# Kernel optimization log

Measured on AMD Instinct MI355X. Metric: run time of the kernel, lower is better.

The kernel has to match this reference:

```python
import jax, jax.numpy as jnp
import numpy as np

N = 100000
E = 1600000
GENE = 512
HID = 128
NCLS = 10
EPS = 1e-5  # BatchNorm1d default eps


def setup_inputs() -> dict:
    key = jax.random.key(0)
    ks = jax.random.split(key, 16)
    def lin(k, fan_in, fan_out):
        return (jax.random.normal(k, (fan_in, fan_out), jnp.float32) / np.sqrt(fan_in)).astype(jnp.float32)
    dims = [(GENE, HID), (HID, 2 * HID), (2 * HID, HID), (HID, HID // 2)]
    inp = {}
    inp["x"] = jax.random.normal(ks[0], (N, GENE), jnp.float32)
    inp["edge_index"] = jax.random.randint(ks[1], (2, E), 0, N)
    for i, (di, do) in enumerate(dims, start=1):
        inp[f"W{i}"] = lin(ks[1 + i], di, do)
        inp[f"b{i}"] = jnp.zeros((do,), jnp.float32)
        inp[f"g{i}"] = jnp.ones((do,), jnp.float32)     # BN gamma
        inp[f"beta{i}"] = jnp.zeros((do,), jnp.float32)  # BN beta
    inp["Wc"] = lin(ks[10], HID // 2, NCLS)
    inp["bc"] = jnp.zeros((NCLS,), jnp.float32)
    return inp


def gcn_conv(h_in, W, b, src, dst, deg_inv_sqrt):
    # PyG GCNConv: transform, then symmetric-normalized aggregation with self-loops
    h = h_in @ W                                   # [N, out]
    norm = (deg_inv_sqrt[src] * deg_inv_sqrt[dst])[:, None]  # [E, 1]
    agg = jnp.zeros_like(h).at[dst].add(h[src] * norm)       # scatter-add over edges
    agg = agg + h * (deg_inv_sqrt ** 2)[:, None]   # self-loop contribution (norm = 1/deg)
    return agg + b


def relu_bn(h, g, beta):
    # forward applies BatchNorm1d(F.relu(h)) in training mode (batch stats, biased var)
    h = jax.nn.relu(h)
    mu = h.mean(axis=0)
    var = h.var(axis=0)
    return (h - mu) * jax.lax.rsqrt(var + EPS) * g + beta


def reference(x, edge_index, W1, b1, g1, beta1, W2, b2, g2, beta2,
              W3, b3, g3, beta3, W4, b4, g4, beta4, Wc, bc):
    src, dst = edge_index[0], edge_index[1]
    # degree after adding self-loops (edge weight 1)
    deg = jnp.zeros((x.shape[0],), x.dtype).at[dst].add(1.0) + 1.0
    dis = jax.lax.rsqrt(deg)
    h = relu_bn(gcn_conv(x, W1, b1, src, dst, dis), g1, beta1)
    h = relu_bn(gcn_conv(h, W2, b2, src, dst, dis), g2, beta2)
    h = relu_bn(gcn_conv(h, W3, b3, src, dst, dis), g3, beta3)
    h = relu_bn(gcn_conv(h, W4, b4, src, dst, dis), g4, beta4)
    return h @ Wc + bc
```

## Files before the change

### kernel.cpp

```cpp
#include <hip/hip_runtime.h>
#include <hip/hip_bf16.h>

#define EPS_BN 1e-5f

using frag8 = __attribute__((ext_vector_type(8))) short;
using f32x4 = __attribute__((ext_vector_type(4))) float;

typedef const __attribute__((address_space(1))) void* gas_ptr;
typedef __attribute__((address_space(3))) void* las_ptr;

__device__ __forceinline__ void async_ld16(const void* g, void* l) {
  __builtin_amdgcn_global_load_lds((gas_ptr)g, (las_ptr)l, 16, 0, 0);
}

__device__ __forceinline__ float bfu2f(unsigned short u) {
  union { unsigned int i; float f; } c;
  c.i = (unsigned int)u << 16;
  return c.f;
}


__global__ void wtrans1_kernel(const float* __restrict__ W1, __hip_bfloat16* __restrict__ T) {
  int i = blockIdx.x * blockDim.x + threadIdx.x;
  if (i < 512 * 128) {
    int k = i / 128, f = i % 128;
    T[f * 512 + k] = __float2bfloat16(W1[i]);
  }
}

__global__ void scan1_kernel(const int* __restrict__ cnt, int* __restrict__ out,
                             int* __restrict__ bsum, float* __restrict__ dis, int n) {
  __shared__ int sdata[1024];
  int tid = threadIdx.x;
  int i = blockIdx.x * 1024 + tid;
  int v = (i < n) ? cnt[i] : 0;
  if (i < n) dis[i] = rsqrtf((float)v + 1.0f);
  sdata[tid] = v;
  __syncthreads();
  for (int off = 1; off < 1024; off <<= 1) {
    int t = (tid >= off) ? sdata[tid - off] : 0;
    __syncthreads();
    sdata[tid] += t;
    __syncthreads();
  }
  if (i < n) out[i] = sdata[tid] - v;
  if (tid == 1023) bsum[blockIdx.x] = sdata[1023];
}

__global__ void scan2_kernel(int* __restrict__ bsum, int nb) {
  __shared__ int sdata[1024];
  int tid = threadIdx.x;
  int v = (tid < nb) ? bsum[tid] : 0;
  sdata[tid] = v;
  __syncthreads();
  for (int off = 1; off < 1024; off <<= 1) {
    int t = (tid >= off) ? sdata[tid - off] : 0;
    __syncthreads();
    sdata[tid] += t;
    __syncthreads();
  }
  if (tid < nb) bsum[tid] = sdata[tid] - v;
}

__global__ void scan3_kernel(int* __restrict__ out, const int* __restrict__ bsum,
                             int n, int E) {
  int i = blockIdx.x * 1024 + threadIdx.x;
  if (i < n) out[i] += bsum[blockIdx.x];
  if (i == 0) out[n] = E;
}

template <int TN, int ASTAGE, int OMODE>
__device__ __forceinline__ void gemm_body(
    const void* __restrict__ Ap, const __hip_bfloat16* __restrict__ Bt,
    __hip_bfloat16* __restrict__ C, const float* __restrict__ bias,
    const float* __restrict__ rowscale,
    const float* __restrict__ statsIn, const float* __restrict__ g,
    const float* __restrict__ beta, float* __restrict__ statsOut, float invN,
    int Nr, int K, int F, int bx, int by) {
  constexpr int WM = (TN == 128) ? 64 : 32;
  constexpr int MI = WM / 16;
  __shared__ __align__(16) __hip_bfloat16 As[128 * 32];
  __shared__ __align__(16) __hip_bfloat16 Bs[TN * 32];
  __shared__ float sacc[128], sqc[128];
  __shared__ float ssc[256], ssb[256];
  int tid = (int)threadIdx.x;
  int wid = tid >> 6, lane = tid & 63;
  int rowBase = bx * 128;
  int colBase = by * TN;
  int wr, wc;
  if (TN == 128) { wr = (wid >> 1) * 64; wc = (wid & 1) * 64; }
  else           { wr = wid * 32;        wc = 0; }

  f32x4 zero = {0.f, 0.f, 0.f, 0.f};
  f32x4 acc[MI][4];
#pragma unroll
  for (int i = 0; i < MI; ++i)
#pragma unroll
    for (int j = 0; j < 4; ++j) acc[i][j] = zero;

  int lm = lane & 15;
  int k8 = (lane >> 4) * 8;

  if constexpr (OMODE == 3) {
    if (tid < 128) { sacc[tid] = 0.f; sqc[tid] = 0.f; }
  }
  if constexpr (ASTAGE == 2) {
    for (int k = tid; k < K; k += 256) {
      float mean = statsIn[k] * invN;
      float var = statsIn[256 + k] * invN - mean * mean;
      float sc = g[k] * rsqrtf(var + EPS_BN);
      ssc[k] = sc;
      ssb[k] = beta[k] - mean * sc;
    }
    __syncthreads();
  }

  for (int k0 = 0; k0 < K; k0 += 32) {
    if constexpr (ASTAGE == 0) {
#pragma unroll
      for (int p = 0; p < 2; ++p) {
        int sidx = p * 256 + tid;
        int row = sidx >> 2;
        int kq = (sidx & 3) * 8;
        int gr = rowBase + row;
        if (gr >= Nr) gr = Nr - 1;
        async_ld16((const __hip_bfloat16*)Ap + (size_t)gr * K + k0 + kq,
                   (char*)As + (p * 256 + wid * 64) * 16);
      }
    } else {
#pragma unroll
      for (int p = 0; p < 2; ++p) {
        int sidx = p * 256 + tid;
        int row = sidx >> 2;
        int kq = (sidx & 3) * 8;
        int gr = rowBase + row;
        if (gr >= Nr) gr = Nr - 1;
        union { frag8 f; __hip_bfloat16 h[8]; } pk;
        if constexpr (ASTAGE == 1) {
          const float* s = (const float*)Ap + (size_t)gr * K + k0 + kq;
          float4 a = *(const float4*)s;
          float4 b2 = *(const float4*)(s + 4);
          pk.h[0] = __float2bfloat16(a.x);  pk.h[1] = __float2bfloat16(a.y);
          pk.h[2] = __float2bfloat16(a.z);  pk.h[3] = __float2bfloat16(a.w);
          pk.h[4] = __float2bfloat16(b2.x); pk.h[5] = __float2bfloat16(b2.y);
          pk.h[6] = __float2bfloat16(b2.z); pk.h[7] = __float2bfloat16(b2.w);
        } else {
          const unsigned short* s = (const unsigned short*)Ap + (size_t)gr * K + k0 + kq;
          ushort4 a = *(const ushort4*)s;
          ushort4 b2 = *(const ushort4*)(s + 4);
          int kk = k0 + kq;
          pk.h[0] = __float2bfloat16(bfu2f(a.x)  * ssc[kk + 0] + ssb[kk + 0]);
          pk.h[1] = __float2bfloat16(bfu2f(a.y)  * ssc[kk + 1] + ssb[kk + 1]);
          pk.h[2] = __float2bfloat16(bfu2f(a.z)  * ssc[kk + 2] + ssb[kk + 2]);
          pk.h[3] = __float2bfloat16(bfu2f(a.w)  * ssc[kk + 3] + ssb[kk + 3]);
          pk.h[4] = __float2bfloat16(bfu2f(b2.x) * ssc[kk + 4] + ssb[kk + 4]);
          pk.h[5] = __float2bfloat16(bfu2f(b2.y) * ssc[kk + 5] + ssb[kk + 5]);
          pk.h[6] = __float2bfloat16(bfu2f(b2.z) * ssc[kk + 6] + ssb[kk + 6]);
          pk.h[7] = __float2bfloat16(bfu2f(b2.w) * ssc[kk + 7] + ssb[kk + 7]);
        }
        *(frag8*)&As[row * 32 + kq] = pk.f;
      }
    }
    constexpr int BPASS = TN / 64;
#pragma unroll
    for (int p = 0; p < BPASS; ++p) {
      int sidx = p * 256 + tid;
      int col = sidx >> 2;
      int kq = (sidx & 3) * 8;
      async_ld16(Bt + (size_t)(colBase + col) * K + k0 + kq,
                 (char*)Bs + (p * 256 + wid * 64) * 16);
    }
    __syncthreads();

    frag8 af[MI], bf[4];
#pragma unroll
    for (int i = 0; i < MI; ++i)
      af[i] = *(const frag8*)&As[(wr + i * 16 + lm) * 32 + k8];
#pragma unroll
    for (int j = 0; j < 4; ++j)
      bf[j] = *(const frag8*)&Bs[(wc + j * 16 + lm) * 32 + k8];
#pragma unroll
    for (int i = 0; i < MI; ++i)
#pragma unroll
      for (int j = 0; j < 4; ++j)
        acc[i][j] = __builtin_amdgcn_mfma_f32_16x16x32_bf16(af[i], bf[j], acc[i][j], 0, 0, 0);
    __syncthreads();
  }

  int rquad = (lane >> 4) * 4;
  float s[4] = {0.f, 0.f, 0.f, 0.f}, q[4] = {0.f, 0.f, 0.f, 0.f};
#pragma unroll
  for (int i = 0; i < MI; ++i) {
    int rb = rowBase + wr + i * 16 + rquad;
#pragma unroll
    for (int r = 0; r < 4; ++r) {
      int row = rb + r;
      if (row < Nr) {
        if constexpr (OMODE == 0) {
#pragma unroll
          for (int j = 0; j < 4; ++j) {
            int col = colBase + wc + j * 16 + lm;
            C[(size_t)row * F + col] = __float2bfloat16(acc[i][j][r]);
          }
        } else if constexpr (OMODE == 1) {
          float rs = rowscale[row];
#pragma unroll
          for (int j = 0; j < 4; ++j) {
            int col = colBase + wc + j * 16 + lm;
            C[(size_t)row * F + col] = __float2bfloat16(acc[i][j][r] * rs);
          }
        } else {
#pragma unroll
          for (int j = 0; j < 4; ++j) {
            int col = colBase + wc + j * 16 + lm;
            float v = acc[i][j][r] + bias[col];
            float rl = fmaxf(v, 0.f);
            C[(size_t)row * F + col] = __float2bfloat16(rl);
            s[j] += rl;
            q[j] += rl * rl;
          }
        }
      }
    }
  }

  if constexpr (OMODE == 3) {
#pragma unroll
    for (int j = 0; j < 4; ++j) {
      s[j] += __shfl_xor(s[j], 16, 64); s[j] += __shfl_xor(s[j], 32, 64);
      q[j] += __shfl_xor(q[j], 16, 64); q[j] += __shfl_xor(q[j], 32, 64);
    }
    if (lane < 16) {
#pragma unroll
      for (int j = 0; j < 4; ++j) {
        atomicAdd(&sacc[wc + j * 16 + lane], s[j]);
        atomicAdd(&sqc[wc + j * 16 + lane], q[j]);
      }
    }
    __syncthreads();
    if (tid < 128) {
      atomicAdd(&statsOut[colBase + tid], sacc[tid]);
      atomicAdd(&statsOut[256 + colBase + tid], sqc[tid]);
    }
  }
}

__global__ __launch_bounds__(256) void fat1_kernel(
    const float* __restrict__ x, const __hip_bfloat16* __restrict__ Wt0,
    __hip_bfloat16* __restrict__ T1, int Nn, int G1,
    const int* __restrict__ e_dst, int* __restrict__ cnt, int* __restrict__ rank,
    int E, int CB,
    const float* __restrict__ W2, const float* __restrict__ W3, const float* __restrict__ W4,
    __hip_bfloat16* __restrict__ Tw2, __hip_bfloat16* __restrict__ Tw3,
    __hip_bfloat16* __restrict__ Tw4) {
  int b = (int)blockIdx.x;
  if (b < G1) {
    gemm_body<128, 1, 0>(x, Wt0, T1, nullptr, nullptr, nullptr, nullptr, nullptr,
                         nullptr, 0.f, Nn, 512, 128, b, 0);
  } else if (b < G1 + CB) {
    int e = (b - G1) * 256 + (int)threadIdx.x;
    if (e < E) rank[e] = atomicAdd(&cnt[e_dst[e]], 1);
  } else {
    int i = (b - G1 - CB) * 256 + (int)threadIdx.x;
    const float* W; __hip_bfloat16* T; int K, F, base;
    if (i < 32768)       { W = W2; T = Tw2; K = 128; F = 256; base = 0; }
    else if (i < 65536)  { W = W3; T = Tw3; K = 256; F = 128; base = 32768; }
    else if (i < 73728)  { W = W4; T = Tw4; K = 128; F = 64;  base = 65536; }
    else return;
    int j = i - base;
    int k = j / F, f = j % F;
    T[f * K + k] = __float2bfloat16(W[j]);
  }
}

template <int TN, int ASTAGE, int OMODE>
__global__ __launch_bounds__(256) void mfma_gemm_kernel(
    const void* __restrict__ A, const __hip_bfloat16* __restrict__ Bt,
    __hip_bfloat16* __restrict__ C, const float* __restrict__ bias,
    const float* __restrict__ rowscale, const float* __restrict__ statsIn,
    const float* __restrict__ g, const float* __restrict__ beta,
    float* __restrict__ statsOut, float invN, int Nr, int K, int F) {
  gemm_body<TN, ASTAGE, OMODE>(A, Bt, C, bias, rowscale, statsIn, g, beta, statsOut,
                               invN, Nr, K, F, (int)blockIdx.x, (int)blockIdx.y);
}

__global__ __launch_bounds__(256) void fat2_kernel(
    const int* __restrict__ src, const int* __restrict__ dst,
    const int* __restrict__ rowstart, const int* __restrict__ rank,
    int* __restrict__ csr_src, int E) {
  int e = (int)blockIdx.x * 256 + (int)threadIdx.x;
  if (e < E) csr_src[rowstart[dst[e]] + rank[e]] = src[e];
}

template <int VEC, int AMODE>
__global__ __launch_bounds__(256) void agg_kernel(
    const __hip_bfloat16* __restrict__ Ts, const int* __restrict__ rowstart,
    const int* __restrict__ csr_src, const float* __restrict__ dis,
    const float* __restrict__ bias, void* __restrict__ H,
    float* __restrict__ stats, const float* __restrict__ statsIn,
    const float* __restrict__ g, const float* __restrict__ beta,
    float* __restrict__ sd, float invN, int Nn, int F) {
  __shared__ float lsum[512], lqs[512];
  __shared__ float ssc[128], ssb[128];
  int tid = (int)threadIdx.x;
  int wid4 = tid >> 6;
  int lane = tid & 63;
  int off = lane * VEC;
  const unsigned short* Tu = (const unsigned short*)Ts;

  if constexpr (AMODE == 2) {
    if (tid < F) {
      float mean = statsIn[tid] * invN;
      float var = statsIn[256 + tid] * invN - mean * mean;
      float sc = g[tid] * rsqrtf(var + EPS_BN);
      ssc[tid] = sc;
      ssb[tid] = beta[tid] - mean * sc;
    }
    __syncthreads();
  }

  float bj[VEC];
  float s[VEC], q[VEC];
#pragma unroll
  for (int j = 0; j < VEC; ++j) {
    bj[j] = (AMODE == 1 || AMODE == 3 || AMODE == 4) ? bias[off + j] : 0.f;
    s[j] = 0.f; q[j] = 0.f;
  }

  for (int d = blockIdx.x * 4 + wid4; d < Nn; d += gridDim.x * 4) {
    float dd = dis[d];
    float acc[VEC];
    {
      unsigned short r[VEC];
      if constexpr (VEC == 2) *(ushort2*)r = *(const ushort2*)&Tu[(size_t)d * F + off];
      else                    r[0] = Tu[(size_t)d * F + off];
#pragma unroll
      for (int j = 0; j < VEC; ++j) {
        if constexpr (AMODE == 1) acc[j] = bfu2f(r[j]) * dd;
        else                      acc[j] = bfu2f(r[j]);
      }
    }
    float sdacc = dd;

    int e0 = rowstart[d], e1 = rowstart[d + 1];
    for (int e = e0; e < e1; e += 16) {
      int idx[16];
      bool val[16];
#pragma unroll
      for (int p = 0; p < 16; ++p) {
        int ee = e + p;
        val[p] = ee < e1;
        idx[p] = csr_src[val[p] ? ee : e1 - 1];
      }
      unsigned short r[16][VEC];
      float dv[16];
#pragma unroll
      for (int p = 0; p < 16; ++p) {
        if constexpr (VEC == 2) *(ushort2*)r[p] = *(const ushort2*)&Tu[(size_t)idx[p] * F + off];
        else                    r[p][0] = Tu[(size_t)idx[p] * F + off];
        if constexpr (AMODE == 1) dv[p] = dis[idx[p]];
      }
#pragma unroll
      for (int p = 0; p < 16; ++p) {
        if constexpr (AMODE == 1) {
#pragma unroll
          for (int j = 0; j < VEC; ++j) acc[j] += val[p] ? bfu2f(r[p][j]) * dv[p] : 0.f;
          sdacc += val[p] ? dv[p] : 0.f;
        } else {
#pragma unroll
          for (int j = 0; j < VEC; ++j) acc[j] += val[p] ? bfu2f(r[p][j]) : 0.f;
        }
      }
    }

    if constexpr (AMODE == 2) {
      float sdv = sd[d];
      union { ushort2 u; __hip_bfloat16 h[2]; } pk;
      pk.h[0] = __float2bfloat16(dd * (ssc[off + 0] * acc[0] + ssb[off + 0] * sdv));
      pk.h[1] = __float2bfloat16(dd * (ssc[off + 1] * acc[1] + ssb[off + 1] * sdv));
      *(ushort2*)&((__hip_bfloat16*)H)[(size_t)d * F + off] = pk.u;
    } else {
      float rl[VEC];
#pragma unroll
      for (int j = 0; j < VEC; ++j) {
        float v = acc[j] * dd + bj[j];
        rl[j] = fmaxf(v, 0.f);
        s[j] += rl[j];
        q[j] += rl[j] * rl[j];
      }
      if constexpr (AMODE == 1) {
        union { ushort2 u; __hip_bfloat16 h[2]; } pk;
        pk.h[0] = __float2bfloat16(rl[0] * dd);
        pk.h[1] = __float2bfloat16(rl[1] * dd);
        *(ushort2*)&((__hip_bfloat16*)H)[(size_t)d * F + off] = pk.u;
        if (lane == 0) sd[d] = sdacc;
      } else if constexpr (AMODE == 3) {
        union { ushort2 u; __hip_bfloat16 h[2]; } pk;
        pk.h[0] = __float2bfloat16(rl[0]);
        pk.h[1] = __float2bfloat16(rl[1]);
        *(ushort2*)&((__hip_bfloat16*)H)[(size_t)d * F + off] = pk.u;
      } else {
        ((float*)H)[(size_t)d * F + off] = rl[0];
      }
    }
  }

  if constexpr (AMODE != 2) {
#pragma unroll
    for (int j = 0; j < VEC; ++j) {
      lsum[(lane * VEC + j) * 4 + wid4] = s[j];
      lqs[(lane * VEC + j) * 4 + wid4] = q[j];
    }
    __syncthreads();
    int nc = 64 * VEC;
    for (int c = tid; c < nc; c += 256) {
      float a = lsum[c * 4 + 0] + lsum[c * 4 + 1] + lsum[c * 4 + 2] + lsum[c * 4 + 3];
      float b = lqs[c * 4 + 0] + lqs[c * 4 + 1] + lqs[c * 4 + 2] + lqs[c * 4 + 3];
      atomicAdd(&stats[c], a);
      atomicAdd(&stats[256 + c], b);
    }
  }
}

__global__ __launch_bounds__(256) void bnapply_cls_kernel(
    const float* __restrict__ R4, const float* __restrict__ stats,
    const float* __restrict__ g, const float* __restrict__ beta,
    const float* __restrict__ Wc, const float* __restrict__ bc,
    float* __restrict__ out, int Nn, float invN) {
  __shared__ float ssc[64], ssb[64];
  int tid = (int)threadIdx.x;
  if (tid < 64) {
    float mean = stats[tid] * invN;
    float var = stats[256 + tid] * invN - mean * mean;
    float sc = g[tid] * rsqrtf(var + EPS_BN);
    ssc[tid] = sc;
    ssb[tid] = beta[tid] - mean * sc;
  }
  __syncthreads();
  int gt = blockIdx.x * blockDim.x + tid;
  int wid = gt >> 6;
  int lane = tid & 63;
  if (wid >= Nn) return;
  float v = R4[(size_t)wid * 64 + lane];
  float h = v * ssc[lane] + ssb[lane];
#pragma unroll
  for (int c = 0; c < 10; ++c) {
    float p = h * Wc[lane * 10 + c];
#pragma unroll
    for (int off = 32; off > 0; off >>= 1) p += __shfl_down(p, off, 64);
    if (lane == 0) out[(size_t)wid * 10 + c] = p + bc[c];
  }
}


extern "C" void kernel_launch(void* const* d_in, const int* in_sizes, int n_in,
                              void* d_out, int out_size, void* d_ws, size_t ws_size,
                              hipStream_t stream) {
  (void)n_in; (void)out_size; (void)ws_size;
  const float* x    = (const float*)d_in[0];
  const int*   edge = (const int*)d_in[1];
  const int E  = in_sizes[1] / 2;
  const int Nn = in_sizes[0] / 512;
  const int* e_src = edge;
  const int* e_dst = edge + E;

  const float* W[4]  = {(const float*)d_in[2],  (const float*)d_in[6],
                        (const float*)d_in[10], (const float*)d_in[14]};
  const float* bv[4] = {(const float*)d_in[3],  (const float*)d_in[7],
                        (const float*)d_in[11], (const float*)d_in[15]};
  const float* gv[4] = {(const float*)d_in[4],  (const float*)d_in[8],
                        (const float*)d_in[12], (const float*)d_in[16]};
  const float* bt[4] = {(const float*)d_in[5],  (const float*)d_in[9],
                        (const float*)d_in[13], (const float*)d_in[17]};
  const float* Wc = (const float*)d_in[18];
  const float* bc = (const float*)d_in[19];
  float* out = (float*)d_out;

  const float invN = 1.0f / (float)Nn;

  char* p = (char*)d_ws;
  auto alloc = [&](size_t bytes) -> void* {
    void* r = (void*)p;
    p += (bytes + 255) & ~(size_t)255;
    return r;
  };
  int*   cnt      = (int*)alloc((size_t)Nn * 4);
  float* stats    = (float*)alloc(2048 * 4);
  size_t zeroBytes = (size_t)(((size_t)Nn * 4 + 255) & ~(size_t)255) + 2048 * 4;
  int*   rowstart = (int*)alloc((size_t)(Nn + 1) * 4);
  int*   bsum     = (int*)alloc(1024 * 4);
  float* dis      = (float*)alloc((size_t)Nn * 4);
  float* sd       = (float*)alloc((size_t)Nn * 4);
  int*   rank     = (int*)alloc((size_t)E * 4);
  int*   csr_src  = (int*)alloc((size_t)E * 4);
  __hip_bfloat16* Wt0 = (__hip_bfloat16*)alloc(512 * 128 * 2);
  __hip_bfloat16* Wt1 = (__hip_bfloat16*)alloc(128 * 256 * 2);
  __hip_bfloat16* Wt2 = (__hip_bfloat16*)alloc(256 * 128 * 2);
  __hip_bfloat16* Wt3 = (__hip_bfloat16*)alloc(128 * 64 * 2);
  __hip_bfloat16* Ts1 = (__hip_bfloat16*)alloc((size_t)Nn * 128 * 2);
  __hip_bfloat16* R1  = (__hip_bfloat16*)alloc((size_t)Nn * 128 * 2);
  __hip_bfloat16* Tb2 = (__hip_bfloat16*)alloc((size_t)Nn * 128 * 2);
  __hip_bfloat16* R2  = (__hip_bfloat16*)alloc((size_t)Nn * 256 * 2);
  __hip_bfloat16* Ts3 = (__hip_bfloat16*)alloc((size_t)Nn * 128 * 2);
  __hip_bfloat16* R3  = (__hip_bfloat16*)alloc((size_t)Nn * 128 * 2);
  __hip_bfloat16* Ts4 = (__hip_bfloat16*)alloc((size_t)Nn * 64 * 2);
  float*          R4  = (float*)alloc((size_t)Nn * 64 * 4);

  hipMemsetAsync(cnt, 0, zeroBytes, stream);

  wtrans1_kernel<<<(512 * 128 + 255) / 256, 256, 0, stream>>>(W[0], Wt0);

  const int gx = (Nn + 127) / 128;
  const int CB = (E + 255) / 256;
  const int WB = (73728 + 255) / 256;
  fat1_kernel<<<gx + CB + WB, 256, 0, stream>>>(
      x, Wt0, Ts1, Nn, gx, e_dst, cnt, rank, E, CB,
      W[1], W[2], W[3], Wt1, Wt2, Wt3);

  int nb = (Nn + 1023) / 1024;
  scan1_kernel<<<nb, 1024, 0, stream>>>(cnt, rowstart, bsum, dis, Nn);
  scan2_kernel<<<1, 1024, 0, stream>>>(bsum, nb);
  scan3_kernel<<<nb, 1024, 0, stream>>>(rowstart, bsum, Nn, E);

  fat2_kernel<<<CB, 256, 0, stream>>>(e_src, e_dst, rowstart, rank, csr_src, E);

  const int AGG_BLOCKS = 2048;

  agg_kernel<2, 1><<<AGG_BLOCKS, 256, 0, stream>>>(
      Ts1, rowstart, csr_src, dis, bv[0], R1, stats, nullptr, nullptr, nullptr,
      sd, invN, Nn, 128);
  agg_kernel<2, 2><<<AGG_BLOCKS, 256, 0, stream>>>(
      R1, rowstart, csr_src, dis, nullptr, Tb2, nullptr, stats, gv[0], bt[0],
      sd, invN, Nn, 128);
  {
    dim3 g(gx, 2);
    mfma_gemm_kernel<128, 0, 3><<<g, 256, 0, stream>>>(
        Tb2, Wt1, R2, bv[1], nullptr, nullptr, nullptr, nullptr, stats + 512, invN,
        Nn, 128, 256);
  }
  {
    dim3 g(gx, 1);
    mfma_gemm_kernel<128, 2, 1><<<g, 256, 0, stream>>>(
        R2, Wt2, Ts3, nullptr, dis, stats + 512, gv[1], bt[1], nullptr, invN,
        Nn, 256, 128);
  }
  agg_kernel<2, 3><<<AGG_BLOCKS, 256, 0, stream>>>(
      Ts3, rowstart, csr_src, dis, bv[2], R3, stats + 1024, nullptr, nullptr, nullptr,
      nullptr, invN, Nn, 128);
  {
    dim3 g(gx, 1);
    mfma_gemm_kernel<64, 2, 1><<<g, 256, 0, stream>>>(
        R3, Wt3, Ts4, nullptr, dis, stats + 1024, gv[2], bt[2], nullptr, invN,
        Nn, 128, 64);
  }
  agg_kernel<1, 4><<<AGG_BLOCKS, 256, 0, stream>>>(
      Ts4, rowstart, csr_src, dis, bv[3], R4, stats + 1536, nullptr, nullptr, nullptr,
      nullptr, invN, Nn, 64);
  int clsBlocks = (Nn * 64 + 255) / 256;
  bnapply_cls_kernel<<<clsBlocks, 256, 0, stream>>>(R4, stats + 1536, gv[3], bt[3],
                                                    Wc, bc, out, Nn, invN);
}
```

Measured before the change: 940.0 us.

## Double-buffer GEMM shared-memory tiles to overlap next-tile loads with MFMA

Converts the GEMM K-loop into a two-stage software pipeline. As and Bs are now double-buffered, and the loads for tile t+1 are issued before the MFMAs on tile t. Register-staged A tiles (fp32 convert, BN affine) are converted and stored after the compute. The loop drops from two barriers per iteration to one and hoists the address computation out of the loop. In exchange it doubles shared-memory use and adds prefetch registers, which may lower occupancy.

```diff
diff --git a/kernel.cpp b/kernel.cpp
--- a/kernel.cpp
+++ b/kernel.cpp
@@ -79,8 +79,9 @@
     int Nr, int K, int F, int bx, int by) {
   constexpr int WM = (TN == 128) ? 64 : 32;
   constexpr int MI = WM / 16;
-  __shared__ __align__(16) __hip_bfloat16 As[128 * 32];
-  __shared__ __align__(16) __hip_bfloat16 Bs[TN * 32];
+  constexpr int BPASS = TN / 64;
+  __shared__ __align__(16) __hip_bfloat16 As[2][128 * 32];
+  __shared__ __align__(16) __hip_bfloat16 Bs[2][TN * 32];
   __shared__ float sacc[128], sqc[128];
   __shared__ float ssc[256], ssb[256];
   int tid = (int)threadIdx.x;
@@ -101,6 +102,26 @@
   int lm = lane & 15;
   int k8 = (lane >> 4) * 8;
 
+  int arow[2], alrow[2], akq[2], adst[2];
+#pragma unroll
+  for (int p = 0; p < 2; ++p) {
+    int sidx = p * 256 + tid;
+    alrow[p] = sidx >> 2;
+    akq[p] = (sidx & 3) * 8;
+    int gr = rowBase + alrow[p];
+    if (gr >= Nr) gr = Nr - 1;
+    arow[p] = gr;
+    adst[p] = (p * 256 + wid * 64) * 16;
+  }
+  int bcol[BPASS], bkq[BPASS], bdst[BPASS];
+#pragma unroll
+  for (int p = 0; p < BPASS; ++p) {
+    int sidx = p * 256 + tid;
+    bcol[p] = colBase + (sidx >> 2);
+    bkq[p] = (sidx & 3) * 8;
+    bdst[p] = (p * 256 + wid * 64) * 16;
+  }
+
   if constexpr (OMODE == 3) {
     if (tid < 128) { sacc[tid] = 0.f; sqc[tid] = 0.f; }
   }
@@ -115,76 +136,109 @@
     __syncthreads();
   }
 
-  for (int k0 = 0; k0 < K; k0 += 32) {
-    if constexpr (ASTAGE == 0) {
-#pragma unroll
-      for (int p = 0; p < 2; ++p) {
-        int sidx = p * 256 + tid;
-        int row = sidx >> 2;
-        int kq = (sidx & 3) * 8;
-        int gr = rowBase + row;
-        if (gr >= Nr) gr = Nr - 1;
-        async_ld16((const __hip_bfloat16*)Ap + (size_t)gr * K + k0 + kq,
-                   (char*)As + (p * 256 + wid * 64) * 16);
-      }
-    } else {
-#pragma unroll
-      for (int p = 0; p < 2; ++p) {
-        int sidx = p * 256 + tid;
-        int row = sidx >> 2;
-        int kq = (sidx & 3) * 8;
-        int gr = rowBase + row;
-        if (gr >= Nr) gr = Nr - 1;
-        union { frag8 f; __hip_bfloat16 h[8]; } pk;
-        if constexpr (ASTAGE == 1) {
-          const float* s = (const float*)Ap + (size_t)gr * K + k0 + kq;
-          float4 a = *(const float4*)s;
-          float4 b2 = *(const float4*)(s + 4);
-          pk.h[0] = __float2bfloat16(a.x);  pk.h[1] = __float2bfloat16(a.y);
-          pk.h[2] = __float2bfloat16(a.z);  pk.h[3] = __float2bfloat16(a.w);
-          pk.h[4] = __float2bfloat16(b2.x); pk.h[5] = __float2bfloat16(b2.y);
-          pk.h[6] = __float2bfloat16(b2.z); pk.h[7] = __float2bfloat16(b2.w);
-        } else {
-          const unsigned short* s = (const unsigned short*)Ap + (size_t)gr * K + k0 + kq;
-          ushort4 a = *(const ushort4*)s;
-          ushort4 b2 = *(const ushort4*)(s + 4);
-          int kk = k0 + kq;
-          pk.h[0] = __float2bfloat16(bfu2f(a.x)  * ssc[kk + 0] + ssb[kk + 0]);
-          pk.h[1] = __float2bfloat16(bfu2f(a.y)  * ssc[kk + 1] + ssb[kk + 1]);
-          pk.h[2] = __float2bfloat16(bfu2f(a.z)  * ssc[kk + 2] + ssb[kk + 2]);
-          pk.h[3] = __float2bfloat16(bfu2f(a.w)  * ssc[kk + 3] + ssb[kk + 3]);
-          pk.h[4] = __float2bfloat16(bfu2f(b2.x) * ssc[kk + 4] + ssb[kk + 4]);
-          pk.h[5] = __float2bfloat16(bfu2f(b2.y) * ssc[kk + 5] + ssb[kk + 5]);
-          pk.h[6] = __float2bfloat16(bfu2f(b2.z) * ssc[kk + 6] + ssb[kk + 6]);
-          pk.h[7] = __float2bfloat16(bfu2f(b2.w) * ssc[kk + 7] + ssb[kk + 7]);
+  auto cvt_store_f32 = [&](int p, int buf, float4 a, float4 b2) {
+    union { frag8 f; __hip_bfloat16 h[8]; } pk;
+    pk.h[0] = __float2bfloat16(a.x);  pk.h[1] = __float2bfloat16(a.y);
+    pk.h[2] = __float2bfloat16(a.z);  pk.h[3] = __float2bfloat16(a.w);
+    pk.h[4] = __float2bfloat16(b2.x); pk.h[5] = __float2bfloat16(b2.y);
+    pk.h[6] = __float2bfloat16(b2.z); pk.h[7] = __float2bfloat16(b2.w);
+    *(frag8*)&As[buf][alrow[p] * 32 + akq[p]] = pk.f;
+  };
+  auto cvt_store_bn = [&](int p, int buf, int kk, ushort4 a, ushort4 b2) {
+    union { frag8 f; __hip_bfloat16 h[8]; } pk;
+    pk.h[0] = __float2bfloat16(bfu2f(a.x)  * ssc[kk + 0] + ssb[kk + 0]);
+    pk.h[1] = __float2bfloat16(bfu2f(a.y)  * ssc[kk + 1] + ssb[kk + 1]);
+    pk.h[2] = __float2bfloat16(bfu2f(a.z)  * ssc[kk + 2] + ssb[kk + 2]);
+    pk.h[3] = __float2bfloat16(bfu2f(a.w)  * ssc[kk + 3] + ssb[kk + 3]);
+    pk.h[4] = __float2bfloat16(bfu2f(b2.x) * ssc[kk + 4] + ssb[kk + 4]);
+    pk.h[5] = __float2bfloat16(bfu2f(b2.y) * ssc[kk + 5] + ssb[kk + 5]);
+    pk.h[6] = __float2bfloat16(bfu2f(b2.z) * ssc[kk + 6] + ssb[kk + 6]);
+    pk.h[7] = __float2bfloat16(bfu2f(b2.w) * ssc[kk + 7] + ssb[kk + 7]);
+    *(frag8*)&As[buf][alrow[p] * 32 + akq[p]] = pk.f;
+  };
+
+  if constexpr (ASTAGE == 0) {
+#pragma unroll
+    for (int p = 0; p < 2; ++p)
+      async_ld16((const __hip_bfloat16*)Ap + (size_t)arow[p] * K + akq[p],
+                 (char*)As[0] + adst[p]);
+  } else if constexpr (ASTAGE == 1) {
+#pragma unroll
+    for (int p = 0; p < 2; ++p) {
+      const float* s = (const float*)Ap + (size_t)arow[p] * K + akq[p];
+      cvt_store_f32(p, 0, *(const float4*)s, *(const float4*)(s + 4));
+    }
+  } else {
+#pragma unroll
+    for (int p = 0; p < 2; ++p) {
+      const unsigned short* s = (const unsigned short*)Ap + (size_t)arow[p] * K + akq[p];
+      cvt_store_bn(p, 0, akq[p], *(const ushort4*)s, *(const ushort4*)(s + 4));
+    }
+  }
+#pragma unroll
+  for (int p = 0; p < BPASS; ++p)
+    async_ld16(Bt + (size_t)bcol[p] * K + bkq[p], (char*)Bs[0] + bdst[p]);
+  __syncthreads();
+
+  int nt = K >> 5;
+  int cur = 0;
+  for (int t = 0; t < nt; ++t) {
+    int k0n = (t + 1) << 5;
+    bool hasNext = (t + 1) < nt;
+    float4 pf0[2], pf1[2];
+    ushort4 pu0[2], pu1[2];
+
+    if (hasNext) {
+      if constexpr (ASTAGE == 0) {
+#pragma unroll
+        for (int p = 0; p < 2; ++p)
+          async_ld16((const __hip_bfloat16*)Ap + (size_t)arow[p] * K + k0n + akq[p],
+                     (char*)As[cur ^ 1] + adst[p]);
+      } else if constexpr (ASTAGE == 1) {
+#pragma unroll
+        for (int p = 0; p < 2; ++p) {
+          const float* s = (const float*)Ap + (size_t)arow[p] * K + k0n + akq[p];
+          pf0[p] = *(const float4*)s;
+          pf1[p] = *(const float4*)(s + 4);
         }
-        *(frag8*)&As[row * 32 + kq] = pk.f;
-      }
-    }
-    constexpr int BPASS = TN / 64;
-#pragma unroll
-    for (int p = 0; p < BPASS; ++p) {
-      int sidx = p * 256 + tid;
-      int col = sidx >> 2;
-      int kq = (sidx & 3) * 8;
-      async_ld16(Bt + (size_t)(colBase + col) * K + k0 + kq,
-                 (char*)Bs + (p * 256 + wid * 64) * 16);
-    }
-    __syncthreads();
-
-    frag8 af[MI], bf[4];
+      } else {
+#pragma unroll
+        for (int p = 0; p < 2; ++p) {
+          const unsigned short* s =
+              (const unsigned short*)Ap + (size_t)arow[p] * K + k0n + akq[p];
+          pu0[p] = *(const ushort4*)s;
+          pu1[p] = *(const ushort4*)(s + 4);
+        }
+      }
+#pragma unroll
+      for (int p = 0; p < BPASS; ++p)
+        async_ld16(Bt + (size_t)bcol[p] * K + k0n + bkq[p], (char*)Bs[cur ^ 1] + bdst[p]);
+    }
+
+    frag8 af[MI], bfr[4];
 #pragma unroll
     for (int i = 0; i < MI; ++i)
-      af[i] = *(const frag8*)&As[(wr + i * 16 + lm) * 32 + k8];
+      af[i] = *(const frag8*)&As[cur][(wr + i * 16 + lm) * 32 + k8];
 #pragma unroll
     for (int j = 0; j < 4; ++j)
-      bf[j] = *(const frag8*)&Bs[(wc + j * 16 + lm) * 32 + k8];
+      bfr[j] = *(const frag8*)&Bs[cur][(wc + j * 16 + lm) * 32 + k8];
 #pragma unroll
     for (int i = 0; i < MI; ++i)
 #pragma unroll
       for (int j = 0; j < 4; ++j)
-        acc[i][j] = __builtin_amdgcn_mfma_f32_16x16x32_bf16(af[i], bf[j], acc[i][j], 0, 0, 0);
-    __syncthreads();
+        acc[i][j] = __builtin_amdgcn_mfma_f32_16x16x32_bf16(af[i], bfr[j], acc[i][j], 0, 0, 0);
+
+    if (hasNext) {
+      if constexpr (ASTAGE == 1) {
+#pragma unroll
+        for (int p = 0; p < 2; ++p) cvt_store_f32(p, cur ^ 1, pf0[p], pf1[p]);
+      } else if constexpr (ASTAGE == 2) {
+#pragma unroll
+        for (int p = 0; p < 2; ++p) cvt_store_bn(p, cur ^ 1, k0n + akq[p], pu0[p], pu1[p]);
+      }
+    }
+    __syncthreads();
+    cur ^= 1;
   }
 
   int rquad = (lane >> 4) * 4;
```

Result: no change. 942.7 us (+0.3%).
